# Performance work log

Measured on AMD Instinct MI355X. Metric: run time of the kernel, lower is better.

Reference implementation:

```python
import jax, jax.numpy as jnp
import numpy as np
import math

B, T, D = 2, 2048, 512      # batch, n_tp, input_dim
DM, H = 64, 16              # per-head d_model, nhead


def setup_inputs() -> dict:
    key = jax.random.key(0)
    ks = jax.random.split(key, 12)
    s = 0.02
    return {
        "data": jax.random.normal(ks[0], (B, T, D), jnp.float32),
        "mask": jax.random.uniform(ks[1], (B, T, D), jnp.float32),
        "wq": jax.random.normal(ks[2], (D, DM * H), jnp.float32) * s,
        "bq": jnp.zeros((DM * H,), jnp.float32),
        "wk": jax.random.normal(ks[3], (D, DM * H), jnp.float32) * s,
        "bk": jnp.zeros((DM * H,), jnp.float32),
        "wv": jax.random.normal(ks[4], (D, DM * H), jnp.float32) * s,
        "bv": jnp.zeros((DM * H,), jnp.float32),
        "wo": jax.random.normal(ks[5], (DM * H, D), jnp.float32) * s,
        "bo": jnp.zeros((D,), jnp.float32),
    }


def reference(data, mask, wq, bq, wk, bk, wv, bv, wo, bo):
    b, t, d = data.shape
    # NOTE: torch code splits proj as (d_model, nhead): head index is fastest-varying
    def split_heads(x):  # [b,t,DM*H] -> [b,H,t,DM]
        return x.reshape(b, t, DM, H).transpose(0, 3, 1, 2)

    q = split_heads(data @ wq + bq)
    k = split_heads(data @ wk + bk)
    v = split_heads(data @ wv + bv)

    scores = jnp.einsum("bhqd,bhkd->bhqk", q, k) / math.sqrt(DM)
    # padded key positions: rows of mask that sum to exactly 0
    pad = (jnp.sum(mask, axis=-1) == 0.0)  # [b, t] (key axis)
    scores = jnp.where(pad[:, None, None, :], -1e9, scores)
    attn = jax.nn.softmax(scores, axis=-1)  # dropout = identity (eval mode)
    out = jnp.einsum("bhqk,bhkd->bhqd", attn, v)
    # merge as (nhead, d_model) — matches torch permute(0,2,1,3).reshape
    out = out.transpose(0, 2, 1, 3).reshape(b, t, H * DM)
    return out @ wo + bo
```

## Files before the change

kernel.cpp:

```cpp
#include <hip/hip_runtime.h>
#include <hip/hip_bf16.h>

#define B_  2
#define T_  2048
#define D_  512
#define DM_ 64
#define H_  16
#define NQ_ (DM_*H_)
#define NP_ (T_/128)

typedef __bf16 bf16x8 __attribute__((ext_vector_type(8)));
typedef __bf16 bf16x4 __attribute__((ext_vector_type(4)));
typedef float  f32x4  __attribute__((ext_vector_type(4)));
typedef unsigned int u32;

static __device__ __forceinline__ __bf16 bfc(float x) { return (__bf16)x; }
static __device__ __forceinline__ unsigned short f2bf(float x) {
    __bf16 b = (__bf16)x;
    unsigned short u;
    __builtin_memcpy(&u, &b, 2);
    return u;
}
static __device__ __forceinline__ u32 pack2bf(float a, float b) {
    return (u32)f2bf(a) | ((u32)f2bf(b) << 16);
}

#if __has_builtin(__builtin_amdgcn_exp2f)
static __device__ __forceinline__ float EXP2(float x) { return __builtin_amdgcn_exp2f(x); }
#else
static __device__ __forceinline__ float EXP2(float x) {
    float r; asm("v_exp_f32 %0, %1\ns_nop 0" : "=v"(r) : "v"(x)); return r;
}
#endif

#define GLOAD16(gp, lp) \
    __builtin_amdgcn_global_load_lds((const __attribute__((address_space(1))) u32*)(gp), \
                                     (__attribute__((address_space(3))) u32*)(lp), 16, 0, 0)

__global__ __launch_bounds__(256)
void prep_kernel(const float* __restrict__ mask, float* __restrict__ padb,
                 const float* __restrict__ data, unsigned short* __restrict__ dataB,
                 const float* __restrict__ wq, const float* __restrict__ wk,
                 const float* __restrict__ wv, unsigned short* __restrict__ btall,
                 const float* __restrict__ wo, unsigned short* __restrict__ wot)
{
    __shared__ float t[32][33];
    const int bid = blockIdx.x;
    const int tid = threadIdx.x;
    if (bid < 1024) {
        const int row  = bid * 4 + (tid >> 6);
        const int lane = tid & 63;
        const float* p = mask + (size_t)row * D_;
        float4 a = *(const float4*)&p[lane * 8];
        float4 b = *(const float4*)&p[lane * 8 + 4];
        float s = a.x + a.y + a.z + a.w + b.x + b.y + b.z + b.w;
#pragma unroll
        for (int off = 32; off; off >>= 1) s += __shfl_down(s, off);
        if (lane == 0) padb[row] = (s == 0.0f) ? -1e9f : 0.0f;
    } else if (bid < 2048) {
        int i = ((bid - 1024) * 256 + tid) * 8;
        float4 a = *(const float4*)&data[i];
        float4 b = *(const float4*)&data[i + 4];
        bf16x8 u = {bfc(a.x), bfc(a.y), bfc(a.z), bfc(a.w),
                    bfc(b.x), bfc(b.y), bfc(b.z), bfc(b.w)};
        *(bf16x8*)&dataB[i] = u;
    } else if (bid < 3584) {
        const int idx = bid - 2048;
        const int z = idx >> 9, rem = idx & 511;
        const int c0 = (rem & 31) * 32, r0 = (rem >> 5) * 32;
        const float* in = (z == 0) ? wq : (z == 1) ? wk : wv;
        unsigned short* out = btall + (size_t)z * NQ_ * D_;
        const int tx = tid & 31, ty = tid >> 5;
#pragma unroll
        for (int i = 0; i < 4; ++i)
            t[ty * 4 + i][tx] = in[(size_t)(r0 + ty * 4 + i) * NQ_ + c0 + tx];
        __syncthreads();
#pragma unroll
        for (int i = 0; i < 4; ++i) {
            int c  = c0 + ty * 4 + i;
            int rp = (c & 15) * 64 + (c >> 4);
            out[(size_t)rp * D_ + r0 + tx] = f2bf(t[tx][ty * 4 + i]);
        }
    } else {
        const int idx = bid - 3584;
        const int c0 = (idx & 15) * 32, r0 = (idx >> 4) * 32;
        const int tx = tid & 31, ty = tid >> 5;
#pragma unroll
        for (int i = 0; i < 4; ++i)
            t[ty * 4 + i][tx] = wo[(size_t)(r0 + ty * 4 + i) * D_ + c0 + tx];
        __syncthreads();
#pragma unroll
        for (int i = 0; i < 4; ++i)
            wot[(size_t)(c0 + ty * 4 + i) * NQ_ + r0 + tx] = f2bf(t[tx][ty * 4 + i]);
    }
}

__global__ __launch_bounds__(256)
void mgemm_qkv_kernel(const unsigned short* __restrict__ A,
                      const unsigned short* __restrict__ BtAll,
                      const float* __restrict__ bq, const float* __restrict__ bk,
                      const float* __restrict__ bv,
                      unsigned short* __restrict__ Qh, unsigned short* __restrict__ Kh,
                      unsigned short* __restrict__ Vt, float alpha_q)
{
    const int K = D_;
    __shared__ __align__(16) unsigned short Al[2][128 * 64];
    __shared__ __align__(16) unsigned short Bl[2][128 * 64];

    const int tid = threadIdx.x;
    const int w  = tid >> 6, l = tid & 63;
    const int lo = l & 15,  g = l >> 4;
    const int wri = w >> 1, wci = w & 1;
    const int m0 = blockIdx.y * 128, n0 = blockIdx.x * 128;
    const int lrow = l >> 3;
    const int lslot = (l & 7) ^ lrow;

    f32x4 acc[4][4] = {};
    const int nk = K >> 6;

#pragma unroll
    for (int p = 0; p < 4; ++p) {
        int br = w * 32 + p * 8;
        GLOAD16(A     + (size_t)(m0 + br + lrow) * K + lslot * 8, (char*)Al[0] + br * 128);
        GLOAD16(BtAll + (size_t)(n0 + br + lrow) * K + lslot * 8, (char*)Bl[0] + br * 128);
    }
    __syncthreads();

    for (int t = 0; t < nk; ++t) {
        const int cur = t & 1;
        if (t + 1 < nk) {
            const int k0 = (t + 1) << 6;
#pragma unroll
            for (int p = 0; p < 4; ++p) {
                int br = w * 32 + p * 8;
                GLOAD16(A     + (size_t)(m0 + br + lrow) * K + k0 + lslot * 8,
                        (char*)Al[cur ^ 1] + br * 128);
                GLOAD16(BtAll + (size_t)(n0 + br + lrow) * K + k0 + lslot * 8,
                        (char*)Bl[cur ^ 1] + br * 128);
            }
        }
#pragma unroll
        for (int kk = 0; kk < 2; ++kk) {
            bf16x8 af[4], bfr[4];
#pragma unroll
            for (int i = 0; i < 4; ++i) {
                int row = wri * 64 + i * 16 + lo;
                af[i] = *(const bf16x8*)&Al[cur][row * 64 + ((((kk << 2) + g) ^ (row & 7)) << 3)];
                int col = wci * 64 + i * 16 + lo;
                bfr[i] = *(const bf16x8*)&Bl[cur][col * 64 + ((((kk << 2) + g) ^ (col & 7)) << 3)];
            }
#pragma unroll
            for (int i = 0; i < 4; ++i)
#pragma unroll
                for (int j = 0; j < 4; ++j)
                    acc[i][j] = __builtin_amdgcn_mfma_f32_16x16x32_bf16(af[i], bfr[j], acc[i][j], 0, 0, 0);
        }
        __syncthreads();
    }

    const int seg = n0 >> 10;
    const int n0l = n0 & 1023;
    const float* bias = (seg == 0) ? bq : (seg == 1) ? bk : bv;
    const float alpha = (seg == 0) ? alpha_q : 1.0f;
    const int h = (n0l >> 6) + wci;

    float bb[4];
#pragma unroll
    for (int j = 0; j < 4; ++j) bb[j] = bias[(j * 16 + lo) * 16 + h];

    const int mb_l = wri * 64 + g * 4;
    if (seg < 2) {
        unsigned short* o16 = (seg == 0) ? Qh : Kh;
        unsigned short* hb = (unsigned short*)Al + wci * (128 * 64);
#pragma unroll
        for (int i = 0; i < 4; ++i)
#pragma unroll
            for (int jj = 0; jj < 4; ++jj) {
                int ml = mb_l + i * 16 + jj;
#pragma unroll
                for (int j = 0; j < 4; ++j) {
                    int dm = j * 16 + lo;
                    int off = ml * 64 + (((dm >> 3) ^ (ml & 7)) << 3) + (dm & 7);
                    hb[off] = f2bf((acc[i][j][jj] + bb[j]) * alpha);
                }
            }
        __syncthreads();
        const int rrow = l >> 3, rch = l & 7;
#pragma unroll
        for (int p = 0; p < 8; ++p) {
            int ml = wri * 64 + p * 8 + rrow;
            bf16x8 v = *(const bf16x8*)&hb[ml * 64 + (((rch ^ (ml & 7))) << 3)];
            int m = m0 + ml;
            int t = m & (T_ - 1), bidx = m >> 11;
            *(bf16x8*)&o16[(((size_t)(bidx * H_ + h)) * T_ + t) * DM_ + rch * 8] = v;
        }
    } else {
#pragma unroll
        for (int i = 0; i < 4; ++i)
#pragma unroll
            for (int j = 0; j < 4; ++j) {
                int m = m0 + mb_l + i * 16;
                int t = m & (T_ - 1), bidx = m >> 11;
                int dm = j * 16 + lo;
                bf16x4 u = {bfc(acc[i][j][0] + bb[j]), bfc(acc[i][j][1] + bb[j]),
                            bfc(acc[i][j][2] + bb[j]), bfc(acc[i][j][3] + bb[j])};
                *(bf16x4*)&Vt[((size_t)(bidx * H_ + h) * DM_ + dm) * T_ + t] = u;
            }
    }
}

__global__ __launch_bounds__(256)
void mgemm_out_kernel(const unsigned short* __restrict__ A,
                      const unsigned short* __restrict__ Bt,
                      const float* __restrict__ bias, float* __restrict__ out,
                      int M, int N, int K)
{
    __shared__ __align__(16) unsigned short Al[2][64 * 64];
    __shared__ __align__(16) unsigned short Bl[2][128 * 64];

    const int tid = threadIdx.x;
    const int w  = tid >> 6, l = tid & 63;
    const int lo = l & 15,  g = l >> 4;
    const int wri = w >> 1, wci = w & 1;
    const int m0 = blockIdx.y * 64, n0 = blockIdx.x * 128;
    const int lrow = l >> 3;
    const int lslot = (l & 7) ^ lrow;

    f32x4 acc[2][4] = {};
    const int nk = K >> 6;

#pragma unroll
    for (int p = 0; p < 2; ++p) {
        int br = w * 16 + p * 8;
        GLOAD16(A + (size_t)(m0 + br + lrow) * K + lslot * 8, (char*)Al[0] + br * 128);
    }
#pragma unroll
    for (int p = 0; p < 4; ++p) {
        int br = w * 32 + p * 8;
        GLOAD16(Bt + (size_t)(n0 + br + lrow) * K + lslot * 8, (char*)Bl[0] + br * 128);
    }
    __syncthreads();

    for (int t = 0; t < nk; ++t) {
        const int cur = t & 1;
        if (t + 1 < nk) {
            const int k0 = (t + 1) << 6;
#pragma unroll
            for (int p = 0; p < 2; ++p) {
                int br = w * 16 + p * 8;
                GLOAD16(A + (size_t)(m0 + br + lrow) * K + k0 + lslot * 8,
                        (char*)Al[cur ^ 1] + br * 128);
            }
#pragma unroll
            for (int p = 0; p < 4; ++p) {
                int br = w * 32 + p * 8;
                GLOAD16(Bt + (size_t)(n0 + br + lrow) * K + k0 + lslot * 8,
                        (char*)Bl[cur ^ 1] + br * 128);
            }
        }
#pragma unroll
        for (int kk = 0; kk < 2; ++kk) {
            bf16x8 af[2], bfr[4];
#pragma unroll
            for (int i = 0; i < 2; ++i) {
                int row = wri * 32 + i * 16 + lo;
                af[i] = *(const bf16x8*)&Al[cur][row * 64 + ((((kk << 2) + g) ^ (row & 7)) << 3)];
            }
#pragma unroll
            for (int j = 0; j < 4; ++j) {
                int col = wci * 64 + j * 16 + lo;
                bfr[j] = *(const bf16x8*)&Bl[cur][col * 64 + ((((kk << 2) + g) ^ (col & 7)) << 3)];
            }
#pragma unroll
            for (int i = 0; i < 2; ++i)
#pragma unroll
                for (int j = 0; j < 4; ++j)
                    acc[i][j] = __builtin_amdgcn_mfma_f32_16x16x32_bf16(af[i], bfr[j], acc[i][j], 0, 0, 0);
        }
        __syncthreads();
    }

    const int mb = m0 + wri * 32 + g * 4;
#pragma unroll
    for (int j = 0; j < 4; ++j) {
        int n = n0 + wci * 64 + j * 16 + lo;
        float bb = bias[n];
#pragma unroll
        for (int i = 0; i < 2; ++i)
#pragma unroll
            for (int jj = 0; jj < 4; ++jj) {
                int m = mb + i * 16 + jj;
                out[(size_t)m * N + n] = acc[i][j][jj] + bb;
            }
    }
}

__global__ __launch_bounds__(256, 2)
void attn_kernel(const unsigned short* __restrict__ Qh,
                 const unsigned short* __restrict__ Kh,
                 const unsigned short* __restrict__ Vt,
                 const float* __restrict__ padb,
                 unsigned short* __restrict__ ctx)
{
    __shared__ __align__(16) unsigned short Ks[4][64 * 64];
    __shared__ __align__(16) unsigned short Vs[4][64 * 64];
    __shared__ __align__(16) float pbs[T_];

    const int tid  = threadIdx.x;
    const int w    = tid >> 6;
    const int l    = tid & 63;
    const int lo16 = l & 15;
    const int g    = l >> 4;
    const int lrow = l >> 3;
    const int lslot = (l & 7) ^ lrow;

    const int f   = blockIdx.x;
    const int s   = f >> 3;
    const int bh  = (f & 7) * 4 + (s >> 4);
    const int q0  = (s & 15) * 128;
    const int bb  = bh >> 4;
    const int hh  = bh & 15;

    bf16x8 qf[2][2];
#pragma unroll
    for (int qt = 0; qt < 2; ++qt) {
        const unsigned short* Qp =
            Qh + ((size_t)bh * T_ + q0 + w * 32 + qt * 16 + lo16) * DM_ + g * 8;
        qf[qt][0] = *(const bf16x8*)(Qp);
        qf[qt][1] = *(const bf16x8*)(Qp + 32);
    }

    const unsigned short* kgp =
        Kh + (size_t)bh * T_ * DM_ + (size_t)(w * 16 + lrow) * DM_ + lslot * 8;
    const unsigned short* vgp =
        Vt + (size_t)bh * DM_ * T_ + (size_t)(w * 16 + lrow) * T_ + lslot * 8;

    {
        const float* src = padb + bb * T_ + tid * 8;
        *(float4*)&pbs[tid * 8]     = *(const float4*)(src);
        *(float4*)&pbs[tid * 8 + 4] = *(const float4*)(src + 4);
    }

    GLOAD16(kgp,                (char*)Ks[0] + (w * 16) * 128);
    GLOAD16(kgp + 8 * DM_,      (char*)Ks[0] + (w * 16 + 8) * 128);
    GLOAD16(kgp + 64 * DM_,     (char*)Ks[1] + (w * 16) * 128);
    GLOAD16(kgp + 72 * DM_,     (char*)Ks[1] + (w * 16 + 8) * 128);
    GLOAD16(vgp,                (char*)Vs[0] + (w * 16) * 128);
    GLOAD16(vgp + 8 * T_,       (char*)Vs[0] + (w * 16 + 8) * 128);
    GLOAD16(vgp + 64,           (char*)Vs[1] + (w * 16) * 128);
    GLOAD16(vgp + 8 * T_ + 64,  (char*)Vs[1] + (w * 16 + 8) * 128);
    kgp += 128 * DM_;
    vgp += 128;
    __syncthreads();

    f32x4 oa[2][4] = {};
    f32x4 ls4[2] = {};

    char* KrA = (char*)Ks[0]; char* KrB = (char*)Ks[1];
    char* KwA = (char*)Ks[2]; char* KwB = (char*)Ks[3];
    char* VrA = (char*)Vs[0]; char* VrB = (char*)Vs[1];
    char* VwA = (char*)Vs[2]; char* VwB = (char*)Vs[3];

    auto process = [&](const char* Kt, const char* Vc, int pboff) {
        f32x4 sa[2][4];
#pragma unroll
        for (int nt = 0; nt < 4; ++nt) {
            f32x4 pb4 = *(const f32x4*)&pbs[pboff + nt * 16 + g * 4];
            sa[0][nt] = pb4;
            sa[1][nt] = pb4;
        }
        __builtin_amdgcn_s_setprio(1);
#pragma unroll
        for (int ks = 0; ks < 2; ++ks) {
#pragma unroll
            for (int nt = 0; nt < 4; ++nt) {
                int row = nt * 16 + lo16;
                int off = (row * 128 + ks * 64 + g * 16) ^ ((row & 7) << 4);
                bf16x8 kf = *(const bf16x8*)(Kt + off);
#pragma unroll
                for (int qt = 0; qt < 2; ++qt)
                    sa[qt][nt] = __builtin_amdgcn_mfma_f32_16x16x32_bf16(kf, qf[qt][ks], sa[qt][nt], 0, 0, 0);
            }
        }
        __builtin_amdgcn_s_setprio(0);

        u32 pw[2][4][2];
#pragma unroll
        for (int qt = 0; qt < 2; ++qt)
#pragma unroll
            for (int nt = 0; nt < 4; ++nt) {
                float e0 = EXP2(sa[qt][nt][0]);
                float e1 = EXP2(sa[qt][nt][1]);
                float e2 = EXP2(sa[qt][nt][2]);
                float e3 = EXP2(sa[qt][nt][3]);
                ls4[qt] += (f32x4){e0, e1, e2, e3};
                pw[qt][nt][0] = pack2bf(e0, e1);
                pw[qt][nt][1] = pack2bf(e2, e3);
            }
        bf16x8 pf[2][2];
#pragma unroll
        for (int qt = 0; qt < 2; ++qt)
#pragma unroll
            for (int ks = 0; ks < 2; ++ks) {
                uint4 uu;
                uu.x = pw[qt][2 * ks][0];
                uu.y = pw[qt][2 * ks][1];
                uu.z = pw[qt][2 * ks + 1][0];
                uu.w = pw[qt][2 * ks + 1][1];
                pf[qt][ks] = *(const bf16x8*)&uu;
            }

        __builtin_amdgcn_s_setprio(1);
#pragma unroll
        for (int ks = 0; ks < 2; ++ks)
#pragma unroll
            for (int nd = 0; nd < 4; ++nd) {
                int row = nd * 16 + lo16;
                int sw = (row & 7) << 4;
                int o0 = (row * 128 + ks * 64 + g * 8) ^ sw;
                int o1 = (row * 128 + ks * 64 + 32 + g * 8) ^ sw;
                uint2 a = *(const uint2*)(Vc + o0);
                uint2 b = *(const uint2*)(Vc + o1);
                uint4 uu; uu.x = a.x; uu.y = a.y; uu.z = b.x; uu.w = b.y;
                bf16x8 vf = *(const bf16x8*)&uu;
#pragma unroll
                for (int qt = 0; qt < 2; ++qt)
                    oa[qt][nd] = __builtin_amdgcn_mfma_f32_16x16x32_bf16(vf, pf[qt][ks], oa[qt][nd], 0, 0, 0);
            }
        __builtin_amdgcn_s_setprio(0);
    };

    for (int p = 0; p < NP_; ++p) {
        if (p + 1 < NP_) {
            GLOAD16(kgp,               KwA + (w * 16) * 128);
            GLOAD16(kgp + 8 * DM_,     KwA + (w * 16 + 8) * 128);
            GLOAD16(kgp + 64 * DM_,    KwB + (w * 16) * 128);
            GLOAD16(kgp + 72 * DM_,    KwB + (w * 16 + 8) * 128);
            GLOAD16(vgp,               VwA + (w * 16) * 128);
            GLOAD16(vgp + 8 * T_,      VwA + (w * 16 + 8) * 128);
            GLOAD16(vgp + 64,          VwB + (w * 16) * 128);
            GLOAD16(vgp + 8 * T_ + 64, VwB + (w * 16 + 8) * 128);
            kgp += 128 * DM_;
            vgp += 128;
        }

        process(KrA, VrA, p * 128);
        process(KrB, VrB, p * 128 + 64);

        __syncthreads();
        { char* t0;
          t0 = KrA; KrA = KwA; KwA = t0;
          t0 = KrB; KrB = KwB; KwB = t0;
          t0 = VrA; VrA = VwA; VwA = t0;
          t0 = VrB; VrB = VwB; VwB = t0; }
    }

#pragma unroll
    for (int qt = 0; qt < 2; ++qt) {
        float lt = (ls4[qt][0] + ls4[qt][1]) + (ls4[qt][2] + ls4[qt][3]);
        lt += __shfl_xor(lt, 16);
        lt += __shfl_xor(lt, 32);
        float linv = 1.0f / lt;
        const size_t crow =
            ((size_t)(bb * T_ + q0 + w * 32 + qt * 16 + lo16)) * NQ_ + hh * DM_;
#pragma unroll
        for (int nd = 0; nd < 4; ++nd) {
            bf16x4 u = {bfc(oa[qt][nd][0] * linv), bfc(oa[qt][nd][1] * linv),
                        bfc(oa[qt][nd][2] * linv), bfc(oa[qt][nd][3] * linv)};
            *(bf16x4*)&ctx[crow + nd * 16 + g * 4] = u;
        }
    }
}

extern "C" void kernel_launch(void* const* d_in, const int* in_sizes, int n_in,
                              void* d_out, int out_size, void* d_ws, size_t ws_size,
                              hipStream_t stream) {
    const float* data = (const float*)d_in[0];
    const float* mask = (const float*)d_in[1];
    const float* wq   = (const float*)d_in[2];
    const float* bq   = (const float*)d_in[3];
    const float* wk   = (const float*)d_in[4];
    const float* bk   = (const float*)d_in[5];
    const float* wv   = (const float*)d_in[6];
    const float* bv   = (const float*)d_in[7];
    const float* wo   = (const float*)d_in[8];
    const float* bo   = (const float*)d_in[9];
    float* out = (float*)d_out;

    char* ws = (char*)d_ws;
    const size_t MB = 1024 * 1024;
    unsigned short* Qh    = (unsigned short*)(ws);
    unsigned short* Kh    = (unsigned short*)(ws +  8 * MB);
    unsigned short* Vt    = (unsigned short*)(ws + 16 * MB);
    unsigned short* CTX   = (unsigned short*)(ws + 24 * MB);
    unsigned short* dataB = (unsigned short*)(ws + 32 * MB);
    unsigned short* BtAll = (unsigned short*)(ws + 36 * MB);
    unsigned short* wot   = (unsigned short*)(ws + 39 * MB);
    float*          padb  = (float*)         (ws + 40 * MB);

    const int M = B_ * T_;
    const float alpha_q = 0.125f * 1.44269504089f;

    prep_kernel<<<4096, 256, 0, stream>>>(mask, padb, data, dataB,
                                          wq, wk, wv, BtAll, wo, wot);

    mgemm_qkv_kernel<<<dim3(3 * NQ_ / 128, M / 128), 256, 0, stream>>>(
        dataB, BtAll, bq, bk, bv, Qh, Kh, Vt, alpha_q);

    attn_kernel<<<512, 256, 0, stream>>>(Qh, Kh, Vt, padb, CTX);

    mgemm_out_kernel<<<dim3(D_ / 128, M / 64), 256, 0, stream>>>(
        CTX, wot, bo, out, M, D_, NQ_);
}
```

Measured before the change: 98.82 us.

## Halve attention block to 2 waves with 64-query tiles and 64-key double buffering

The attention kernel now launches 1024 blocks of 128 threads, each covering 64 queries instead of 128. The K/V staging in shared memory shrinks from four 64-key buffers (two 128-key stages) to two 64-key buffers with a simple ping-pong per 64-key tile. The goal is more blocks for better CU balance and occupancy, and a smaller LDS footprint per block. In exchange, K/V tiles are loaded twice as often overall, and there are twice as many barriers per unit of work.

```diff
diff --git a/kernel.cpp b/kernel.cpp
--- a/kernel.cpp
+++ b/kernel.cpp
@@ -7,7 +7,7 @@
 #define DM_ 64
 #define H_  16
 #define NQ_ (DM_*H_)
-#define NP_ (T_/128)
+#define NT_ (T_/64)
 
 typedef __bf16 bf16x8 __attribute__((ext_vector_type(8)));
 typedef __bf16 bf16x4 __attribute__((ext_vector_type(4)));
@@ -295,15 +295,15 @@
     }
 }
 
-__global__ __launch_bounds__(256, 2)
+__global__ __launch_bounds__(128, 2)
 void attn_kernel(const unsigned short* __restrict__ Qh,
                  const unsigned short* __restrict__ Kh,
                  const unsigned short* __restrict__ Vt,
                  const float* __restrict__ padb,
                  unsigned short* __restrict__ ctx)
 {
-    __shared__ __align__(16) unsigned short Ks[4][64 * 64];
-    __shared__ __align__(16) unsigned short Vs[4][64 * 64];
+    __shared__ __align__(16) unsigned short Ks[2][64 * 64];
+    __shared__ __align__(16) unsigned short Vs[2][64 * 64];
     __shared__ __align__(16) float pbs[T_];
 
     const int tid  = threadIdx.x;
@@ -316,8 +316,8 @@
 
     const int f   = blockIdx.x;
     const int s   = f >> 3;
-    const int bh  = (f & 7) * 4 + (s >> 4);
-    const int q0  = (s & 15) * 128;
+    const int bh  = (f & 7) * 4 + (s >> 5);
+    const int q0  = (s & 31) * 64;
     const int bb  = bh >> 4;
     const int hh  = bh & 15;
 
@@ -331,41 +331,47 @@
     }
 
     const unsigned short* kgp =
-        Kh + (size_t)bh * T_ * DM_ + (size_t)(w * 16 + lrow) * DM_ + lslot * 8;
+        Kh + (size_t)bh * T_ * DM_ + (size_t)(w * 32 + lrow) * DM_ + lslot * 8;
     const unsigned short* vgp =
-        Vt + (size_t)bh * DM_ * T_ + (size_t)(w * 16 + lrow) * T_ + lslot * 8;
+        Vt + (size_t)bh * DM_ * T_ + (size_t)(w * 32 + lrow) * T_ + lslot * 8;
 
     {
-        const float* src = padb + bb * T_ + tid * 8;
-        *(float4*)&pbs[tid * 8]     = *(const float4*)(src);
-        *(float4*)&pbs[tid * 8 + 4] = *(const float4*)(src + 4);
-    }
-
-    GLOAD16(kgp,                (char*)Ks[0] + (w * 16) * 128);
-    GLOAD16(kgp + 8 * DM_,      (char*)Ks[0] + (w * 16 + 8) * 128);
-    GLOAD16(kgp + 64 * DM_,     (char*)Ks[1] + (w * 16) * 128);
-    GLOAD16(kgp + 72 * DM_,     (char*)Ks[1] + (w * 16 + 8) * 128);
-    GLOAD16(vgp,                (char*)Vs[0] + (w * 16) * 128);
-    GLOAD16(vgp + 8 * T_,       (char*)Vs[0] + (w * 16 + 8) * 128);
-    GLOAD16(vgp + 64,           (char*)Vs[1] + (w * 16) * 128);
-    GLOAD16(vgp + 8 * T_ + 64,  (char*)Vs[1] + (w * 16 + 8) * 128);
-    kgp += 128 * DM_;
-    vgp += 128;
+        const float* src = padb + bb * T_ + tid * 16;
+#pragma unroll
+        for (int i = 0; i < 4; ++i)
+            *(float4*)&pbs[tid * 16 + i * 4] = *(const float4*)(src + i * 4);
+    }
+
+#pragma unroll
+    for (int p = 0; p < 4; ++p) {
+        GLOAD16(kgp + p * 8 * DM_, (char*)Ks[0] + (w * 32 + p * 8) * 128);
+        GLOAD16(vgp + p * 8 * T_,  (char*)Vs[0] + (w * 32 + p * 8) * 128);
+    }
+    kgp += 64 * DM_;
+    vgp += 64;
     __syncthreads();
 
     f32x4 oa[2][4] = {};
     f32x4 ls4[2] = {};
 
-    char* KrA = (char*)Ks[0]; char* KrB = (char*)Ks[1];
-    char* KwA = (char*)Ks[2]; char* KwB = (char*)Ks[3];
-    char* VrA = (char*)Vs[0]; char* VrB = (char*)Vs[1];
-    char* VwA = (char*)Vs[2]; char* VwB = (char*)Vs[3];
-
-    auto process = [&](const char* Kt, const char* Vc, int pboff) {
+    char* Kr = (char*)Ks[0]; char* Kw = (char*)Ks[1];
+    char* Vr = (char*)Vs[0]; char* Vw = (char*)Vs[1];
+
+    for (int t = 0; t < NT_; ++t) {
+        if (t + 1 < NT_) {
+#pragma unroll
+            for (int p = 0; p < 4; ++p) {
+                GLOAD16(kgp + p * 8 * DM_, Kw + (w * 32 + p * 8) * 128);
+                GLOAD16(vgp + p * 8 * T_,  Vw + (w * 32 + p * 8) * 128);
+            }
+            kgp += 64 * DM_;
+            vgp += 64;
+        }
+
         f32x4 sa[2][4];
 #pragma unroll
         for (int nt = 0; nt < 4; ++nt) {
-            f32x4 pb4 = *(const f32x4*)&pbs[pboff + nt * 16 + g * 4];
+            f32x4 pb4 = *(const f32x4*)&pbs[t * 64 + nt * 16 + g * 4];
             sa[0][nt] = pb4;
             sa[1][nt] = pb4;
         }
@@ -376,7 +382,7 @@
             for (int nt = 0; nt < 4; ++nt) {
                 int row = nt * 16 + lo16;
                 int off = (row * 128 + ks * 64 + g * 16) ^ ((row & 7) << 4);
-                bf16x8 kf = *(const bf16x8*)(Kt + off);
+                bf16x8 kf = *(const bf16x8*)(Kr + off);
 #pragma unroll
                 for (int qt = 0; qt < 2; ++qt)
                     sa[qt][nt] = __builtin_amdgcn_mfma_f32_16x16x32_bf16(kf, qf[qt][ks], sa[qt][nt], 0, 0, 0);
@@ -419,8 +425,8 @@
                 int sw = (row & 7) << 4;
                 int o0 = (row * 128 + ks * 64 + g * 8) ^ sw;
                 int o1 = (row * 128 + ks * 64 + 32 + g * 8) ^ sw;
-                uint2 a = *(const uint2*)(Vc + o0);
-                uint2 b = *(const uint2*)(Vc + o1);
+                uint2 a = *(const uint2*)(Vr + o0);
+                uint2 b = *(const uint2*)(Vr + o1);
                 uint4 uu; uu.x = a.x; uu.y = a.y; uu.z = b.x; uu.w = b.y;
                 bf16x8 vf = *(const bf16x8*)&uu;
 #pragma unroll
@@ -428,31 +434,10 @@
                     oa[qt][nd] = __builtin_amdgcn_mfma_f32_16x16x32_bf16(vf, pf[qt][ks], oa[qt][nd], 0, 0, 0);
             }
         __builtin_amdgcn_s_setprio(0);
-    };
-
-    for (int p = 0; p < NP_; ++p) {
-        if (p + 1 < NP_) {
-            GLOAD16(kgp,               KwA + (w * 16) * 128);
-            GLOAD16(kgp + 8 * DM_,     KwA + (w * 16 + 8) * 128);
-            GLOAD16(kgp + 64 * DM_,    KwB + (w * 16) * 128);
-            GLOAD16(kgp + 72 * DM_,    KwB + (w * 16 + 8) * 128);
-            GLOAD16(vgp,               VwA + (w * 16) * 128);
-            GLOAD16(vgp + 8 * T_,      VwA + (w * 16 + 8) * 128);
-            GLOAD16(vgp + 64,          VwB + (w * 16) * 128);
-            GLOAD16(vgp + 8 * T_ + 64, VwB + (w * 16 + 8) * 128);
-            kgp += 128 * DM_;
-            vgp += 128;
-        }
-
-        process(KrA, VrA, p * 128);
-        process(KrB, VrB, p * 128 + 64);
-
-        __syncthreads();
-        { char* t0;
-          t0 = KrA; KrA = KwA; KwA = t0;
-          t0 = KrB; KrB = KwB; KwB = t0;
-          t0 = VrA; VrA = VwA; VwA = t0;
-          t0 = VrB; VrB = VwB; VwB = t0; }
+
+        __syncthreads();
+        { char* t0 = Kr; Kr = Kw; Kw = t0;
+          char* t1 = Vr; Vr = Vw; Vw = t1; }
     }
 
 #pragma unroll
@@ -507,7 +492,7 @@
     mgemm_qkv_kernel<<<dim3(3 * NQ_ / 128, M / 128), 256, 0, stream>>>(
         dataB, BtAll, bq, bk, bv, Qh, Kh, Vt, alpha_q);
 
-    attn_kernel<<<512, 256, 0, stream>>>(Qh, Kh, Vt, padb, CTX);
+    attn_kernel<<<1024, 128, 0, stream>>>(Qh, Kh, Vt, padb, CTX);
 
     mgemm_out_kernel<<<dim3(D_ / 128, M / 64), 256, 0, stream>>>(
         CTX, wot, bo, out, M, D_, NQ_);
```

Result: slower. 100.9 us (+2.1%).
